# Optimization experiments

Hardware: AMD Instinct MI355X
Metric: run time of the kernel (lower is better)

Reference implementation:

```python
import jax, jax.numpy as jnp
import numpy as np

N, E = 20000, 320000
IN_DIM = OUT_DIM = E_IN = E_OUT = 128
BN_EPS = 1e-5

def _lrelu(x):
    return jnp.where(x >= 0, x, 0.1 * x)

def setup_inputs() -> dict:
    key = jax.random.key(0)
    ks = jax.random.split(key, 12)
    def w(k, shape):
        return jax.random.normal(k, shape, jnp.float32) * (shape[0] ** -0.5)
    return {
        "h": jax.random.normal(ks[0], (N, IN_DIM), jnp.float32),
        "edge_w": jax.random.normal(ks[1], (E, E_IN), jnp.float32),
        "W_node": w(ks[2], (IN_DIM, OUT_DIM)),
        "W_eedge": w(ks[3], (E_IN, E_IN)),
        "W_esf": w(ks[4], (E_IN, 1)),
        "W_fuse": w(ks[5], (2 * OUT_DIM + E_IN, OUT_DIM)),
        "b_fuse": jnp.zeros((OUT_DIM,), jnp.float32),
        "W_attn": w(ks[6], (OUT_DIM, 1)),
        "W_conc": w(ks[7], (2 * OUT_DIM + E_IN, OUT_DIM)),
        "b_conc": jnp.zeros((OUT_DIM,), jnp.float32),
        "bn_gamma": jnp.ones((E_IN,), jnp.float32),
        "bn_beta": jnp.zeros((E_IN,), jnp.float32),
        "W_aggre": w(ks[8], (2 * OUT_DIM + 2 * E_IN, E_OUT)),
        "src": jax.random.randint(ks[9], (E,), 0, N),
        "dst": jax.random.randint(ks[10], (E,), 0, N),
    }

def reference(h, edge_w, W_node, W_eedge, W_esf, W_fuse, b_fuse, W_attn,
              W_conc, b_conc, bn_gamma, bn_beta, W_aggre, src, dst):
    # eval mode: dropout = identity, BatchNorm uses running stats (mean 0, var 1)
    hn = h @ W_node                       # embed_node -> ndata['h'] = ndata['oh']
    # self_attention: ow = embed_edge(w); w = edge_sf_atten(lrelu(ow)) * ow
    ow = edge_w @ W_eedge                 # [E, e_in]
    w1 = (_lrelu(ow) @ W_esf) * ow        # [E, e_in]
    # inter_attention
    hs, hd = hn[src], hn[dst]             # [E, out]
    sat = jnp.concatenate([hs, hd, w1], axis=-1)          # [E, 2*out+e_in]
    inw = _lrelu(sat @ W_fuse + b_fuse)                   # [E, out]
    a = inw @ W_attn                                      # [E, 1]
    w2 = a * w1                                           # edata['w']
    # reduce_func2: segment softmax over incoming edges (grouped by dst)
    s = a[:, 0]
    m = jax.ops.segment_max(s, dst, num_segments=N)
    e = jnp.exp(s - m[dst])
    denom = jax.ops.segment_sum(e, dst, num_segments=N)
    alpha = (e / denom[dst])[:, None]                     # [E, 1]
    t = jnp.concatenate([hs, w2], axis=-1)                # [E, out+e_in]
    h_agg = jax.ops.segment_sum(alpha * t, dst, num_segments=N)  # [N, out+e_in]
    h_new = jnp.concatenate([h_agg, hn], axis=-1) @ W_conc + b_conc
    # DGL only updates nodes that received messages; zero-indegree keep embed_node(h)
    indeg = jax.ops.segment_sum(jnp.ones((E,), jnp.float32), dst, num_segments=N)
    h_out = jnp.where(indeg[:, None] > 0, h_new, hn)      # [N, out]
    # edge_calc: BN(w2) then aggre_embed_edge(cat(src_h, dst_h, bn_w, ow))
    w_bn = (w2 / jnp.sqrt(jnp.float32(1.0) + BN_EPS)) * bn_gamma + bn_beta
    z = jnp.concatenate([h_out[src], h_out[dst], w_bn, ow], axis=-1)
    w_out = z @ W_aggre                                   # [E, e_out]
    return h_out, w_out, sat
```

## Files before the change

### kernel.cpp

```cpp
#include <hip/hip_runtime.h>
#include <hip/hip_bf16.h>

#define TB 256
#define TBM 512
#define BM 64
#define BK 32
#define BN 128
#define ASTR 68
#define MAXD 160

static constexpr int NN = 20000;
static constexpr int NE = 320000;
static constexpr int NB = 313;

static constexpr long long OFF_OW  = 0;
static constexpr long long OFF_HN  = 40960000;
static constexpr long long OFF_PQ  = 43520000;
static constexpr long long OFF_S   = 48640000;
static constexpr long long OFF_DEN = 48960000;
static constexpr long long OFF_CUR = 48980000;
static constexpr long long OFF_WT  = 49000000;
static constexpr long long WS_FLOATS = 49100000;

static constexpr int U_EH = 0;
static constexpr int U_EL = 16384;
static constexpr int U_FH = 32768;
static constexpr int U_FL = 81920;
static constexpr int U_AH = 131072;
static constexpr int U_AL = 163840;

static constexpr long long OUT_HOUT = 0;
static constexpr long long OUT_WOUT = 2560000;
static constexpr long long OUT_SAT  = 43520000;

typedef __attribute__((ext_vector_type(8))) short s8v;
typedef __attribute__((ext_vector_type(4))) float f32x4;
typedef __attribute__((ext_vector_type(8))) unsigned short u16x8;
typedef __attribute__((ext_vector_type(4))) unsigned short u16x4;

#define MFMA16(a,b,c) __builtin_amdgcn_mfma_f32_16x16x32_bf16(a,b,c,0,0,0)

__device__ __forceinline__ float lrelu(float x){ return x >= 0.f ? x : 0.1f*x; }

__device__ __forceinline__ void gl16(const void* g, void* l){
    __builtin_amdgcn_global_load_lds(
        (const __attribute__((address_space(1))) void*)g,
        (__attribute__((address_space(3))) void*)l, 16, 0, 0);
}

__device__ __forceinline__ void split1(float f, unsigned short& hi, unsigned short& lo){
    __hip_bfloat16 h = __float2bfloat16(f);
    float hf = __bfloat162float(h);
    __hip_bfloat16 l = __float2bfloat16(f - hf);
    hi = __builtin_bit_cast(unsigned short, h);
    lo = __builtin_bit_cast(unsigned short, l);
}
__device__ __forceinline__ void split8(float4 a, float4 b, s8v& hi, s8v& lo){
    float v[8] = {a.x,a.y,a.z,a.w,b.x,b.y,b.z,b.w};
#pragma unroll
    for (int j = 0; j < 8; ++j){
        unsigned short hs, ls;
        split1(v[j], hs, ls);
        hi[j] = (short)hs; lo[j] = (short)ls;
    }
}
__device__ __forceinline__ float bfp(unsigned p){
    return __uint_as_float(p & 0xffff0000u) + __uint_as_float(p << 16);
}

__device__ __forceinline__ int lds_a(int row, int g){
    return row*32 + ((g ^ (row & 3)) << 3);
}

__device__ __forceinline__ void store_At(float (*Ast)[ASTR], int k4, int r, float4 v){
    Ast[k4+0][r] = v.x; Ast[k4+1][r] = v.y; Ast[k4+2][r] = v.z; Ast[k4+3][r] = v.w;
}
__device__ __forceinline__ void mm_chunk(const float (*Ast)[ASTR], const float (*Bs)[BN],
                                         int r0, int c0, float acc[4][8]){
#pragma unroll 4
    for (int k = 0; k < BK; ++k){
        const float4 av = *(const float4*)&Ast[k][r0];
        const float4 b0 = *(const float4*)&Bs[k][c0];
        const float4 b1 = *(const float4*)&Bs[k][64 + c0];
        const float a0=av.x, a1=av.y, a2=av.z, a3=av.w;
        const float b[8] = {b0.x,b0.y,b0.z,b0.w,b1.x,b1.y,b1.z,b1.w};
#pragma unroll
        for (int j = 0; j < 8; ++j){
            acc[0][j] = fmaf(a0, b[j], acc[0][j]);
            acc[1][j] = fmaf(a1, b[j], acc[1][j]);
            acc[2][j] = fmaf(a2, b[j], acc[2][j]);
            acc[3][j] = fmaf(a3, b[j], acc[3][j]);
        }
    }
}
__device__ __forceinline__ void load_B(const float* __restrict__ W, int kc,
                                       float (*Bs)[BN], int tid){
#pragma unroll
    for (int p = 0; p < 4; ++p){
        int idx = p*TB + tid;
        int row = idx >> 5;
        int c4  = (idx & 31) << 2;
        *(float4*)&Bs[row][c4] = *(const float4*)&W[(size_t)(kc+row)*BN + c4];
    }
}

__global__ __launch_bounds__(TB) void k_prep(const float* __restrict__ We,
                                             const float* __restrict__ Wf,
                                             const float* __restrict__ Wa,
                                             unsigned short* __restrict__ wt,
                                             int* __restrict__ cur){
    int id = blockIdx.x*TB + threadIdx.x;
    if (id < NN) cur[id] = 0;
    unsigned short hs, ls;
    if (id < 16384){
        int n = id >> 7, k = id & 127;
        split1(We[(size_t)k*128 + n], hs, ls);
        wt[U_EH + id] = hs; wt[U_EL + id] = ls;
    } else if (id < 65536){
        int local = id - 16384;
        int n = local / 384, k = local - n*384;
        split1(Wf[(size_t)k*128 + n], hs, ls);
        wt[U_FH + local] = hs; wt[U_FL + local] = ls;
    } else if (id < 98304){
        int local = id - 65536;
        int n = local >> 8, kk = local & 255;
        split1(Wa[(size_t)(256+kk)*128 + n], hs, ls);
        wt[U_AH + local] = hs; wt[U_AL + local] = ls;
    }
}

__global__ __launch_bounds__(TB) void kB_count(const int* __restrict__ dst,
                                               int* __restrict__ cur){
    int e = blockIdx.x*TB + threadIdx.x;
    atomicAdd(&cur[dst[e]], 1);
}
__global__ __launch_bounds__(TB) void kC_scan(int* __restrict__ cur,
                                              int* __restrict__ offs){
    __shared__ int part[TB];
    __shared__ int spre[TB];
    const int tid = threadIdx.x;
    const int CH = (NN + TB - 1) / TB;
    const int base = tid * CH;
    int sum = 0;
    for (int i = 0; i < CH; ++i){ int idx = base + i; if (idx < NN) sum += cur[idx]; }
    part[tid] = sum;
    __syncthreads();
    if (tid == 0){ int r = 0; for (int i = 0; i < TB; ++i){ spre[i] = r; r += part[i]; } }
    __syncthreads();
    int run = spre[tid];
    for (int i = 0; i < CH; ++i){
        int idx = base + i;
        if (idx < NN){ int c = cur[idx]; offs[idx] = run; cur[idx] = run; run += c; }
    }
}
__global__ __launch_bounds__(TB) void kD_scatter(const int* __restrict__ dst,
                                                 int* __restrict__ cur,
                                                 int* __restrict__ eidx){
    int e = blockIdx.x*TB + threadIdx.x;
    int p = atomicAdd(&cur[dst[e]], 1);
    eidx[p] = e;
}

__global__ __launch_bounds__(TB) void k1_hn(const float* __restrict__ h,
                                            const float* __restrict__ Wn,
                                            unsigned short* __restrict__ hnH,
                                            unsigned short* __restrict__ hnL,
                                            unsigned* __restrict__ hnP){
    __shared__ float Ast[BK][ASTR];
    __shared__ float Bs[BK][BN];
    const int tid = threadIdx.x;
    const int rbase = blockIdx.x * BM;
    const int tc = tid & 15, tr = tid >> 4;
    const int r0 = tr*4, c0 = tc*4;
    float acc[4][8] = {};
    for (int kc = 0; kc < 128; kc += BK){
        __syncthreads();
        {
            int lr = tid >> 3, k4 = (tid & 7) << 2;
#pragma unroll
            for (int p = 0; p < 2; ++p){
                int r = p*32 + lr;
                int rr = rbase + r; if (rr >= NN) rr = NN-1;
                float4 v = *(const float4*)&h[(size_t)rr*128 + kc + k4];
                store_At(Ast, k4, r, v);
            }
        }
        load_B(Wn, kc, Bs, tid);
        __syncthreads();
        mm_chunk(Ast, Bs, r0, c0, acc);
    }
#pragma unroll
    for (int i = 0; i < 4; ++i){
        int rr = rbase + r0 + i;
        if (rr < NN){
            u16x4 h0, l0, h1, l1;
            uint4 p0, p1;
#pragma unroll
            for (int j = 0; j < 4; ++j){
                unsigned short hs, ls;
                split1(acc[i][j], hs, ls);
                h0[j] = hs; l0[j] = ls;
                ((unsigned*)&p0)[j] = ((unsigned)hs << 16) | ls;
                split1(acc[i][4+j], hs, ls);
                h1[j] = hs; l1[j] = ls;
                ((unsigned*)&p1)[j] = ((unsigned)hs << 16) | ls;
            }
            *(u16x4*)&hnH[(size_t)rr*128 + c0] = h0;
            *(u16x4*)&hnL[(size_t)rr*128 + c0] = l0;
            *(u16x4*)&hnH[(size_t)rr*128 + 64 + c0] = h1;
            *(u16x4*)&hnL[(size_t)rr*128 + 64 + c0] = l1;
            *(uint4*)&hnP[(size_t)rr*128 + c0] = p0;
            *(uint4*)&hnP[(size_t)rr*128 + 64 + c0] = p1;
        }
    }
}


__global__ __launch_bounds__(TBM) void k2_mfma(const float* __restrict__ ew,
                                               const unsigned short* __restrict__ wtH,
                                               const unsigned short* __restrict__ wtL,
                                               const float* __restrict__ Wesf,
                                               unsigned short* __restrict__ owH,
                                               unsigned short* __restrict__ owL,
                                               float* __restrict__ sat){
    __shared__ __align__(16) unsigned short Ah[2][4096], Al[2][4096], Bh[2][4096], Bl[2][4096];
    __shared__ float sEsf[128];
    const int tid = threadIdx.x;
    const long long rbase = (long long)blockIdx.x * 128;
    const int lane = tid & 63, w = tid >> 6;
    const int ls = lane & 15, lg = lane >> 4;
    const int srow = tid >> 2, sg = tid & 3;
    const int gsw = sg ^ (srow & 3);
    const int aslot = srow*32 + (gsw << 3);
    if (tid < 128) sEsf[tid] = Wesf[tid];
    f32x4 acc[8] = {};
    auto stage = [&](int nb, int t){
        const int kc = t*32;
        gl16(&wtH[srow*128 + kc + gsw*8], &Bh[nb][w*512]);
        gl16(&wtL[srow*128 + kc + gsw*8], &Bl[nb][w*512]);
        const float* p = &ew[(rbase + srow)*128 + kc + sg*8];
        float4 v0 = *(const float4*)p, v1 = *(const float4*)(p+4);
        s8v hi, lo; split8(v0, v1, hi, lo);
        *(s8v*)&Ah[nb][aslot] = hi; *(s8v*)&Al[nb][aslot] = lo;
    };
    stage(0, 0);
    __syncthreads();
    int cur = 0;
    for (int t = 0; t < 4; ++t){
        if (t+1 < 4) stage(cur^1, t+1);
        s8v ah = *(const s8v*)&Ah[cur][lds_a(w*16 + ls, lg)];
        s8v al = *(const s8v*)&Al[cur][lds_a(w*16 + ls, lg)];
#pragma unroll
        for (int ct = 0; ct < 8; ++ct){
            int c = ct*16 + ls;
            s8v bh = *(const s8v*)&Bh[cur][lds_a(c,lg)];
            s8v bl = *(const s8v*)&Bl[cur][lds_a(c,lg)];
            acc[ct] = MFMA16(ah, bh, acc[ct]);
            acc[ct] = MFMA16(ah, bl, acc[ct]);
            acc[ct] = MFMA16(al, bh, acc[ct]);
        }
        __syncthreads();
        cur ^= 1;
    }
#pragma unroll
    for (int reg = 0; reg < 4; ++reg){
        float p = 0.f;
#pragma unroll
        for (int ct = 0; ct < 8; ++ct)
            p += lrelu(acc[ct][reg]) * sEsf[ct*16 + ls];
#pragma unroll
        for (int m = 1; m < 16; m <<= 1) p += __shfl_xor(p, m);
        long long orow = rbase + w*16 + lg*4 + reg;
#pragma unroll
        for (int ct = 0; ct < 8; ++ct){
            float o = acc[ct][reg];
            int col = ct*16 + ls;
            sat[orow*384 + 256 + col] = p * o;
            unsigned short hs_, ls_; split1(o, hs_, ls_);
            owH[orow*128 + col] = hs_;
            owL[orow*128 + col] = ls_;
        }
    }
}

__global__ __launch_bounds__(TBM) void k3_mfma(const unsigned short* __restrict__ hnH,
                                               const unsigned short* __restrict__ hnL,
                                               const unsigned* __restrict__ hnP,
                                               const unsigned short* __restrict__ wtH,
                                               const unsigned short* __restrict__ wtL,
                                               const float* __restrict__ bf,
                                               const float* __restrict__ Wattn,
                                               const int* __restrict__ src,
                                               const int* __restrict__ dst,
                                               float* __restrict__ sat,
                                               float* __restrict__ s_ws){
    __shared__ __align__(16) unsigned short Ah[2][4096], Al[2][4096], Bh[2][4096], Bl[2][4096];
    __shared__ float sBf[128], sAtt[128];
    __shared__ int sSrc[128], sDst[128];
    const int tid = threadIdx.x;
    const long long rbase = (long long)blockIdx.x * 128;
    const int lane = tid & 63, w = tid >> 6;
    const int ls = lane & 15, lg = lane >> 4;
    const int srow = tid >> 2, sg = tid & 3;
    const int gsw = sg ^ (srow & 3);
    const int aslot = srow*32 + (gsw << 3);
    if (tid < 128){
        sBf[tid] = bf[tid]; sAtt[tid] = Wattn[tid];
        sSrc[tid] = src[rbase + tid]; sDst[tid] = dst[rbase + tid];
    }
    __syncthreads();
    f32x4 acc[8] = {};
    auto stage = [&](int nb, int t){
        const int kc = t*32;
        gl16(&wtH[srow*384 + kc + gsw*8], &Bh[nb][w*512]);
        gl16(&wtL[srow*384 + kc + gsw*8], &Bl[nb][w*512]);
        long long e = rbase + srow;
        if (kc < 256){
            int node = (kc < 128) ? sSrc[srow] : sDst[srow];
            int col0 = kc & 127;
            gl16(&hnH[(size_t)node*128 + col0 + gsw*8], &Ah[nb][w*512]);
            gl16(&hnL[(size_t)node*128 + col0 + gsw*8], &Al[nb][w*512]);
            const unsigned* pp = &hnP[(size_t)node*128 + col0 + sg*8];
            uint4 q0 = *(const uint4*)pp, q1 = *(const uint4*)(pp+4);
            float4 v0 = {bfp(q0.x), bfp(q0.y), bfp(q0.z), bfp(q0.w)};
            float4 v1 = {bfp(q1.x), bfp(q1.y), bfp(q1.z), bfp(q1.w)};
            *(float4*)&sat[e*384 + kc + sg*8] = v0;
            *(float4*)&sat[e*384 + kc + sg*8 + 4] = v1;
        } else {
            const float* p = &sat[e*384 + kc + sg*8];
            float4 v0 = *(const float4*)p, v1 = *(const float4*)(p+4);
            s8v hi, lo; split8(v0, v1, hi, lo);
            *(s8v*)&Ah[nb][aslot] = hi; *(s8v*)&Al[nb][aslot] = lo;
        }
    };
    stage(0, 0);
    __syncthreads();
    int cur = 0;
    for (int t = 0; t < 12; ++t){
        if (t+1 < 12) stage(cur^1, t+1);
        s8v ah = *(const s8v*)&Ah[cur][lds_a(w*16 + ls, lg)];
        s8v al = *(const s8v*)&Al[cur][lds_a(w*16 + ls, lg)];
#pragma unroll
        for (int ct = 0; ct < 8; ++ct){
            int c = ct*16 + ls;
            s8v bh = *(const s8v*)&Bh[cur][lds_a(c,lg)];
            s8v bl = *(const s8v*)&Bl[cur][lds_a(c,lg)];
            acc[ct] = MFMA16(ah, bh, acc[ct]);
            acc[ct] = MFMA16(ah, bl, acc[ct]);
            acc[ct] = MFMA16(al, bh, acc[ct]);
        }
        __syncthreads();
        cur ^= 1;
    }
#pragma unroll
    for (int reg = 0; reg < 4; ++reg){
        float p = 0.f;
#pragma unroll
        for (int ct = 0; ct < 8; ++ct){
            int col = ct*16 + ls;
            p += lrelu(acc[ct][reg] + sBf[col]) * sAtt[col];
        }
#pragma unroll
        for (int m = 1; m < 16; m <<= 1) p += __shfl_xor(p, m);
        if (ls == 0) s_ws[rbase + w*16 + lg*4 + reg] = p;
    }
}

__global__ __launch_bounds__(TB) void k5_agg(const float* __restrict__ s,
                                             const unsigned* __restrict__ hnP,
                                             const float* __restrict__ sat,
                                             const int* __restrict__ src,
                                             const int* __restrict__ eidx,
                                             const int* __restrict__ offs,
                                             const int* __restrict__ cur,
                                             float* __restrict__ hagg,
                                             float* __restrict__ den){
    __shared__ int   sEu[4][MAXD];
    __shared__ int   sEs[4][MAXD];
    __shared__ float sAl[4][MAXD];
    __shared__ float sWc[4][MAXD];
    const int wv = threadIdx.x >> 6, lane = threadIdx.x & 63;
    const int n = blockIdx.x*4 + wv;
    int* Eu = sEu[wv]; int* Es = sEs[wv];
    float* Al = sAl[wv]; float* Wc = sWc[wv];
    const int start = offs[n];
    const int deg = cur[n] - start;
    const int dc = deg < MAXD ? deg : MAXD;
    for (int i = lane; i < dc; i += 64) Eu[i] = eidx[start+i];
    __syncthreads();
    for (int i = lane; i < dc; i += 64){
        int my = Eu[i], r = 0;
        for (int j = 0; j < dc; ++j) r += (Eu[j] < my);
        Es[r] = my;
    }
    __syncthreads();
    float lm = -3.402823466e38f;
    for (int i = lane; i < dc; i += 64){
        int e = Es[i];
        float sv = s[e];
        Wc[i] = sv;
        Eu[i] = src[e];
        lm = fmaxf(lm, sv);
    }
    for (int i = MAXD + lane; i < deg; i += 64) lm = fmaxf(lm, s[eidx[start+i]]);
#pragma unroll
    for (int m2 = 32; m2; m2 >>= 1) lm = fmaxf(lm, __shfl_xor(lm, m2));
    const float m = lm;
    float lsum = 0.f;
    for (int i = lane; i < dc; i += 64){
        float ev = expf(Wc[i] - m);
        Al[i] = ev;
        lsum += ev;
    }
    for (int i = MAXD + lane; i < deg; i += 64) lsum += expf(s[eidx[start+i]] - m);
#pragma unroll
    for (int m2 = 32; m2; m2 >>= 1) lsum += __shfl_xor(lsum, m2);
    const float denom = lsum;
    const float inv = (deg > 0) ? 1.f/denom : 0.f;
    for (int i = lane; i < dc; i += 64){
        float al = Al[i] * inv;
        Al[i] = al;
        Wc[i] = al * Wc[i];
    }
    __syncthreads();
    float a0=0.f, a1=0.f, a2=0.f, a3=0.f;
    for (int i = 0; i < dc; ++i){
        int sI = Eu[i];
        size_t e = (size_t)Es[i];
        float al = Al[i], wc = Wc[i];
        unsigned p0 = hnP[(size_t)sI*128 + lane];
        unsigned p1 = hnP[(size_t)sI*128 + 64 + lane];
        float w0 = sat[e*384 + 256 + lane];
        float w1v = sat[e*384 + 256 + 64 + lane];
        a0 = fmaf(al, bfp(p0), a0);
        a1 = fmaf(al, bfp(p1), a1);
        a2 = fmaf(wc, w0, a2);
        a3 = fmaf(wc, w1v, a3);
    }
    for (int i = MAXD; i < deg; ++i){
        int e = eidx[start+i];
        float sv = s[e];
        float al = expf(sv - m) * inv;
        float wc = al * sv;
        int sI = src[e];
        a0 = fmaf(al, bfp(hnP[(size_t)sI*128 + lane]), a0);
        a1 = fmaf(al, bfp(hnP[(size_t)sI*128 + 64 + lane]), a1);
        a2 = fmaf(wc, sat[(size_t)e*384 + 256 + lane], a2);
        a3 = fmaf(wc, sat[(size_t)e*384 + 256 + 64 + lane], a3);
    }
    const size_t b = (size_t)n*256;
    hagg[b + lane] = a0;
    hagg[b + 64 + lane] = a1;
    hagg[b + 128 + lane] = a2;
    hagg[b + 192 + lane] = a3;
    if (lane == 0) den[n] = (deg > 0) ? denom : 0.f;
}

__global__ __launch_bounds__(TB) void k6_conc(const float* __restrict__ hagg,
                                              const unsigned* __restrict__ hnP,
                                              const float* __restrict__ Wc,
                                              const float* __restrict__ bc,
                                              const float* __restrict__ den,
                                              float* __restrict__ hout){
    __shared__ float Ast[BK][ASTR];
    __shared__ float Bs[BK][BN];
    __shared__ float sBc[BN];
    const int tid = threadIdx.x;
    const int rbase = blockIdx.x * BM;
    const int tc = tid & 15, tr = tid >> 4;
    const int r0 = tr*4, c0 = tc*4;
    if (tid < BN) sBc[tid] = bc[tid];
    float acc[4][8] = {};
    for (int chunk = 0; chunk < 12; ++chunk){
        int kc = chunk * BK;
        __syncthreads();
        {
            int lr = tid >> 3, k4 = (tid & 7) << 2;
#pragma unroll
            for (int p = 0; p < 2; ++p){
                int r = p*32 + lr;
                int rr = rbase + r; if (rr >= NN) rr = NN-1;
                float4 v;
                if (chunk < 8) v = *(const float4*)&hagg[(size_t)rr*256 + kc + k4];
                else {
                    int cb = (kc - 256) + k4;
                    uint4 q = *(const uint4*)&hnP[(size_t)rr*128 + cb];
                    v.x = bfp(q.x); v.y = bfp(q.y); v.z = bfp(q.z); v.w = bfp(q.w);
                }
                store_At(Ast, k4, r, v);
            }
        }
        load_B(Wc, kc, Bs, tid);
        __syncthreads();
        mm_chunk(Ast, Bs, r0, c0, acc);
    }
#pragma unroll
    for (int i = 0; i < 4; ++i){
        int rr = rbase + r0 + i;
        if (rr >= NN) continue;
        bool keep = den[rr] > 0.f;
        float o[8];
#pragma unroll
        for (int j = 0; j < 8; ++j){
            int col = (j < 4) ? (c0 + j) : (60 + c0 + j);
            float fb = bfp(hnP[(size_t)rr*128 + col]);
            o[j] = keep ? acc[i][j] + sBc[col] : fb;
        }
        float4 o0 = {o[0],o[1],o[2],o[3]}, o1 = {o[4],o[5],o[6],o[7]};
        *(float4*)&hout[(size_t)rr*128 + c0] = o0;
        *(float4*)&hout[(size_t)rr*128 + 64 + c0] = o1;
    }
}

__global__ __launch_bounds__(TB) void kNG(const float* __restrict__ aF,
                                          const float* __restrict__ W,
                                          float* __restrict__ O){
    __shared__ float Ast[BK][ASTR];
    __shared__ float Bs[BK][BN];
    const int tid = threadIdx.x;
    const int half = blockIdx.x >= NB ? 1 : 0;
    const int rbase = (blockIdx.x - half*NB) * BM;
    const float* Wp = W + (size_t)half*16384;
    const int tc = tid & 15, tr = tid >> 4;
    const int r0 = tr*4, c0 = tc*4;
    float acc[4][8] = {};
    for (int kc = 0; kc < 128; kc += BK){
        __syncthreads();
        {
            int lr = tid >> 3, k4 = (tid & 7) << 2;
#pragma unroll
            for (int p = 0; p < 2; ++p){
                int r = p*32 + lr;
                int rr = rbase + r; if (rr >= NN) rr = NN-1;
                float4 v = *(const float4*)&aF[(size_t)rr*128 + kc + k4];
                store_At(Ast, k4, r, v);
            }
        }
        load_B(Wp, kc, Bs, tid);
        __syncthreads();
        mm_chunk(Ast, Bs, r0, c0, acc);
    }
#pragma unroll
    for (int i = 0; i < 4; ++i){
        int rr = rbase + r0 + i;
        if (rr < NN){
            float4 o0 = {acc[i][0],acc[i][1],acc[i][2],acc[i][3]};
            float4 o1 = {acc[i][4],acc[i][5],acc[i][6],acc[i][7]};
            *(float4*)&O[(size_t)rr*256 + half*128 + c0] = o0;
            *(float4*)&O[(size_t)rr*256 + half*128 + 64 + c0] = o1;
        }
    }
}

__global__ __launch_bounds__(TBM) void k7p(const unsigned short* __restrict__ owH,
                                           const unsigned short* __restrict__ owL,
                                           const float* __restrict__ sarr,
                                           const float* __restrict__ sat,
                                           const float* __restrict__ Q,
                                           const float* __restrict__ gamma,
                                           const float* __restrict__ beta,
                                           const unsigned short* __restrict__ wtH,
                                           const unsigned short* __restrict__ wtL,
                                           const int* __restrict__ src,
                                           const int* __restrict__ dst,
                                           float* __restrict__ w2out){
    __shared__ __align__(16) unsigned short Ah[2][4096], Al[2][4096], Bh[2][4096], Bl[2][4096];
    __shared__ float sGam[128], sBet[128], sS[128];
    __shared__ int sSrc[128], sDst[128];
    const int tid = threadIdx.x;
    const long long rbase = (long long)blockIdx.x * 128;
    const int lane = tid & 63, w = tid >> 6;
    const int ls = lane & 15, lg = lane >> 4;
    const int srow = tid >> 2, sg = tid & 3;
    const int gsw = sg ^ (srow & 3);
    const int aslot = srow*32 + (gsw << 3);
    const float ISR = 0.9999950000374997f;
    if (tid < 128){
        sGam[tid] = gamma[tid] * ISR; sBet[tid] = beta[tid];
        sSrc[tid] = src[rbase + tid]; sDst[tid] = dst[rbase + tid];
        sS[tid] = sarr[rbase + tid];
    }
    __syncthreads();
    f32x4 acc[8] = {};
    auto stage = [&](int nb, int t){
        const int kc = t*32;
        gl16(&wtH[srow*256 + kc + gsw*8], &Bh[nb][w*512]);
        gl16(&wtL[srow*256 + kc + gsw*8], &Bl[nb][w*512]);
        long long e = rbase + srow;
        if (kc < 128){
            int cb = kc + sg*8;
            float se = sS[srow];
            const float* p = &sat[e*384 + 256 + cb];
            float4 v0 = *(const float4*)p, v1 = *(const float4*)(p+4);
            v0.x = fmaf(v0.x*se, sGam[cb+0], sBet[cb+0]);
            v0.y = fmaf(v0.y*se, sGam[cb+1], sBet[cb+1]);
            v0.z = fmaf(v0.z*se, sGam[cb+2], sBet[cb+2]);
            v0.w = fmaf(v0.w*se, sGam[cb+3], sBet[cb+3]);
            v1.x = fmaf(v1.x*se, sGam[cb+4], sBet[cb+4]);
            v1.y = fmaf(v1.y*se, sGam[cb+5], sBet[cb+5]);
            v1.z = fmaf(v1.z*se, sGam[cb+6], sBet[cb+6]);
            v1.w = fmaf(v1.w*se, sGam[cb+7], sBet[cb+7]);
            s8v hi, lo; split8(v0, v1, hi, lo);
            *(s8v*)&Ah[nb][aslot] = hi; *(s8v*)&Al[nb][aslot] = lo;
        } else {
            int col0 = kc - 128;
            gl16(&owH[e*128 + col0 + gsw*8], &Ah[nb][w*512]);
            gl16(&owL[e*128 + col0 + gsw*8], &Al[nb][w*512]);
        }
    };
    stage(0, 0);
    __syncthreads();
    int cur = 0;
    for (int t = 0; t < 8; ++t){
        if (t+1 < 8) stage(cur^1, t+1);
        int r = w*16 + ls;
        s8v ah = *(const s8v*)&Ah[cur][r*32 + ((lg ^ (r&3)) << 3)];
        s8v al = *(const s8v*)&Al[cur][r*32 + ((lg ^ (r&3)) << 3)];
#pragma unroll
        for (int ct = 0; ct < 8; ++ct){
            int c = ct*16 + ls;
            s8v bh = *(const s8v*)&Bh[cur][c*32 + ((lg ^ (c&3)) << 3)];
            s8v bl = *(const s8v*)&Bl[cur][c*32 + ((lg ^ (c&3)) << 3)];
            acc[ct] = MFMA16(ah, bh, acc[ct]);
            acc[ct] = MFMA16(ah, bl, acc[ct]);
            acc[ct] = MFMA16(al, bh, acc[ct]);
        }
        __syncthreads();
        cur ^= 1;
    }
#pragma unroll
    for (int reg = 0; reg < 4; ++reg){
        int row = w*16 + lg*4 + reg;
        long long orow = rbase + row;
        int sI = sSrc[row], dI = sDst[row];
#pragma unroll
        for (int ct = 0; ct < 8; ++ct){
            int col = ct*16 + ls;
            w2out[orow*128 + col] = acc[ct][reg]
                                  + Q[(size_t)sI*256 + col]
                                  + Q[(size_t)dI*256 + 128 + col];
        }
    }
}

extern "C" void kernel_launch(void* const* d_in, const int* in_sizes, int n_in,
                              void* d_out, int out_size, void* d_ws, size_t ws_size,
                              hipStream_t stream){
    (void)in_sizes; (void)n_in; (void)out_size;
    const float* h       = (const float*)d_in[0];
    const float* edge_w  = (const float*)d_in[1];
    const float* W_node  = (const float*)d_in[2];
    const float* W_eedge = (const float*)d_in[3];
    const float* W_esf   = (const float*)d_in[4];
    const float* W_fuse  = (const float*)d_in[5];
    const float* b_fuse  = (const float*)d_in[6];
    const float* W_attn  = (const float*)d_in[7];
    const float* W_conc  = (const float*)d_in[8];
    const float* b_conc  = (const float*)d_in[9];
    const float* gamma   = (const float*)d_in[10];
    const float* beta    = (const float*)d_in[11];
    const float* W_aggre = (const float*)d_in[12];
    const int*   src     = (const int*)d_in[13];
    const int*   dst     = (const int*)d_in[14];

    float* out    = (float*)d_out;
    float* o_hout = out + OUT_HOUT;
    float* o_wout = out + OUT_WOUT;
    float* o_sat  = out + OUT_SAT;

    if (ws_size < (size_t)WS_FLOATS * 4) return;
    float* ws     = (float*)d_ws;
    unsigned short* w_owH = (unsigned short*)(ws + OFF_OW);
    unsigned short* w_owL = w_owH + (size_t)NE*128;
    unsigned short* w_hnH = (unsigned short*)(ws + OFF_HN);
    unsigned short* w_hnL = w_hnH + (size_t)NN*128;
    float* w_PQ   = ws + OFF_PQ;
    float* w_s    = ws + OFF_S;
    float* w_den  = ws + OFF_DEN;
    int*   w_cur  = (int*)(ws + OFF_CUR);
    unsigned short* w_wt = (unsigned short*)(ws + OFF_WT);

    unsigned* w_hnP = (unsigned*)o_wout;
    int* w_eidx = (int*)o_hout;
    int* w_offs = w_eidx + NE;

    hipLaunchKernelGGL(k_prep,    dim3(98304/TB), dim3(TB), 0, stream,
                       W_eedge, W_fuse, W_aggre, w_wt, w_cur);
    hipLaunchKernelGGL(kB_count,  dim3(NE/TB), dim3(TB), 0, stream, dst, w_cur);
    hipLaunchKernelGGL(kC_scan,   dim3(1), dim3(TB), 0, stream, w_cur, w_offs);
    hipLaunchKernelGGL(kD_scatter,dim3(NE/TB), dim3(TB), 0, stream, dst, w_cur, w_eidx);
    hipLaunchKernelGGL(k1_hn,     dim3(NB), dim3(TB), 0, stream, h, W_node,
                       w_hnH, w_hnL, w_hnP);
    hipLaunchKernelGGL(k2_mfma,   dim3(NE/128), dim3(TBM), 0, stream, edge_w,
                       w_wt + U_EH, w_wt + U_EL, W_esf, w_owH, w_owL, o_sat);
    hipLaunchKernelGGL(k3_mfma,   dim3(NE/128), dim3(TBM), 0, stream, w_hnH, w_hnL, w_hnP,
                       w_wt + U_FH, w_wt + U_FL, b_fuse, W_attn,
                       src, dst, o_sat, w_s);
    hipLaunchKernelGGL(k5_agg,    dim3(NN/4), dim3(TB), 0, stream, w_s, w_hnP, o_sat,
                       src, w_eidx, w_offs, w_cur, w_PQ, w_den);
    hipLaunchKernelGGL(k6_conc,   dim3(NB), dim3(TB), 0, stream, w_PQ,
                       w_hnP, W_conc, b_conc, w_den, o_hout);
    hipLaunchKernelGGL(kNG,       dim3(2*NB), dim3(TB), 0, stream, o_hout, W_aggre, w_PQ);
    hipLaunchKernelGGL(k7p,       dim3(NE/128), dim3(TBM), 0, stream,
                       w_owH, w_owL, w_s, o_sat, w_PQ, gamma, beta,
                       w_wt + U_AH, w_wt + U_AL, src, dst, o_wout);
}
```

Before: 726.1 us.

## Fuse edge embedding and fuse-attention GEMMs into one kernel, use wave-level syncs

Merges k2 (edge embed and self-attention) and k3 (fuse-layer GEMM and attention score) into a single kernel. The w1 block now feeds the second GEMM straight from registers into LDS instead of being re-read from the sat output in global memory. The K order of the second GEMM is rotated so the w1 chunks come first. In the aggregation kernel, block barriers are replaced with LDS waitcnt, which assumes each wave only touches its own shared slice. The fused kernel holds more registers (acc1, acc2 and pr live together), which may lower occupancy.

```diff
diff --git a/kernel.cpp b/kernel.cpp
--- a/kernel.cpp
+++ b/kernel.cpp
@@ -35,12 +35,13 @@
 
 typedef __attribute__((ext_vector_type(8))) short s8v;
 typedef __attribute__((ext_vector_type(4))) float f32x4;
-typedef __attribute__((ext_vector_type(8))) unsigned short u16x8;
 typedef __attribute__((ext_vector_type(4))) unsigned short u16x4;
 
 #define MFMA16(a,b,c) __builtin_amdgcn_mfma_f32_16x16x32_bf16(a,b,c,0,0,0)
 
 __device__ __forceinline__ float lrelu(float x){ return x >= 0.f ? x : 0.1f*x; }
+
+__device__ __forceinline__ void wsync(){ asm volatile("s_waitcnt lgkmcnt(0)" ::: "memory"); }
 
 __device__ __forceinline__ void gl16(const void* g, void* l){
     __builtin_amdgcn_global_load_lds(
@@ -215,87 +216,25 @@
     }
 }
 
-
-__global__ __launch_bounds__(TBM) void k2_mfma(const float* __restrict__ ew,
-                                               const unsigned short* __restrict__ wtH,
-                                               const unsigned short* __restrict__ wtL,
-                                               const float* __restrict__ Wesf,
-                                               unsigned short* __restrict__ owH,
-                                               unsigned short* __restrict__ owL,
-                                               float* __restrict__ sat){
+__global__ __launch_bounds__(TBM) void k23_mfma(const float* __restrict__ ew,
+                                                const unsigned short* __restrict__ wtEH,
+                                                const unsigned short* __restrict__ wtEL,
+                                                const float* __restrict__ Wesf,
+                                                const unsigned short* __restrict__ wtFH,
+                                                const unsigned short* __restrict__ wtFL,
+                                                const float* __restrict__ bf,
+                                                const float* __restrict__ Wattn,
+                                                const unsigned short* __restrict__ hnH,
+                                                const unsigned short* __restrict__ hnL,
+                                                const unsigned* __restrict__ hnP,
+                                                const int* __restrict__ src,
+                                                const int* __restrict__ dst,
+                                                unsigned short* __restrict__ owH,
+                                                unsigned short* __restrict__ owL,
+                                                float* __restrict__ sat,
+                                                float* __restrict__ s_ws){
     __shared__ __align__(16) unsigned short Ah[2][4096], Al[2][4096], Bh[2][4096], Bl[2][4096];
-    __shared__ float sEsf[128];
-    const int tid = threadIdx.x;
-    const long long rbase = (long long)blockIdx.x * 128;
-    const int lane = tid & 63, w = tid >> 6;
-    const int ls = lane & 15, lg = lane >> 4;
-    const int srow = tid >> 2, sg = tid & 3;
-    const int gsw = sg ^ (srow & 3);
-    const int aslot = srow*32 + (gsw << 3);
-    if (tid < 128) sEsf[tid] = Wesf[tid];
-    f32x4 acc[8] = {};
-    auto stage = [&](int nb, int t){
-        const int kc = t*32;
-        gl16(&wtH[srow*128 + kc + gsw*8], &Bh[nb][w*512]);
-        gl16(&wtL[srow*128 + kc + gsw*8], &Bl[nb][w*512]);
-        const float* p = &ew[(rbase + srow)*128 + kc + sg*8];
-        float4 v0 = *(const float4*)p, v1 = *(const float4*)(p+4);
-        s8v hi, lo; split8(v0, v1, hi, lo);
-        *(s8v*)&Ah[nb][aslot] = hi; *(s8v*)&Al[nb][aslot] = lo;
-    };
-    stage(0, 0);
-    __syncthreads();
-    int cur = 0;
-    for (int t = 0; t < 4; ++t){
-        if (t+1 < 4) stage(cur^1, t+1);
-        s8v ah = *(const s8v*)&Ah[cur][lds_a(w*16 + ls, lg)];
-        s8v al = *(const s8v*)&Al[cur][lds_a(w*16 + ls, lg)];
-#pragma unroll
-        for (int ct = 0; ct < 8; ++ct){
-            int c = ct*16 + ls;
-            s8v bh = *(const s8v*)&Bh[cur][lds_a(c,lg)];
-            s8v bl = *(const s8v*)&Bl[cur][lds_a(c,lg)];
-            acc[ct] = MFMA16(ah, bh, acc[ct]);
-            acc[ct] = MFMA16(ah, bl, acc[ct]);
-            acc[ct] = MFMA16(al, bh, acc[ct]);
-        }
-        __syncthreads();
-        cur ^= 1;
-    }
-#pragma unroll
-    for (int reg = 0; reg < 4; ++reg){
-        float p = 0.f;
-#pragma unroll
-        for (int ct = 0; ct < 8; ++ct)
-            p += lrelu(acc[ct][reg]) * sEsf[ct*16 + ls];
-#pragma unroll
-        for (int m = 1; m < 16; m <<= 1) p += __shfl_xor(p, m);
-        long long orow = rbase + w*16 + lg*4 + reg;
-#pragma unroll
-        for (int ct = 0; ct < 8; ++ct){
-            float o = acc[ct][reg];
-            int col = ct*16 + ls;
-            sat[orow*384 + 256 + col] = p * o;
-            unsigned short hs_, ls_; split1(o, hs_, ls_);
-            owH[orow*128 + col] = hs_;
-            owL[orow*128 + col] = ls_;
-        }
-    }
-}
-
-__global__ __launch_bounds__(TBM) void k3_mfma(const unsigned short* __restrict__ hnH,
-                                               const unsigned short* __restrict__ hnL,
-                                               const unsigned* __restrict__ hnP,
-                                               const unsigned short* __restrict__ wtH,
-                                               const unsigned short* __restrict__ wtL,
-                                               const float* __restrict__ bf,
-                                               const float* __restrict__ Wattn,
-                                               const int* __restrict__ src,
-                                               const int* __restrict__ dst,
-                                               float* __restrict__ sat,
-                                               float* __restrict__ s_ws){
-    __shared__ __align__(16) unsigned short Ah[2][4096], Al[2][4096], Bh[2][4096], Bl[2][4096];
-    __shared__ float sBf[128], sAtt[128];
+    __shared__ float sEsf[128], sBf[128], sAtt[128];
     __shared__ int sSrc[128], sDst[128];
     const int tid = threadIdx.x;
     const long long rbase = (long long)blockIdx.x * 128;
@@ -305,39 +244,24 @@
     const int gsw = sg ^ (srow & 3);
     const int aslot = srow*32 + (gsw << 3);
     if (tid < 128){
-        sBf[tid] = bf[tid]; sAtt[tid] = Wattn[tid];
+        sEsf[tid] = Wesf[tid]; sBf[tid] = bf[tid]; sAtt[tid] = Wattn[tid];
         sSrc[tid] = src[rbase + tid]; sDst[tid] = dst[rbase + tid];
     }
-    __syncthreads();
-    f32x4 acc[8] = {};
-    auto stage = [&](int nb, int t){
+    f32x4 acc1[8] = {};
+    auto stageA = [&](int nb, int t){
         const int kc = t*32;
-        gl16(&wtH[srow*384 + kc + gsw*8], &Bh[nb][w*512]);
-        gl16(&wtL[srow*384 + kc + gsw*8], &Bl[nb][w*512]);
-        long long e = rbase + srow;
-        if (kc < 256){
-            int node = (kc < 128) ? sSrc[srow] : sDst[srow];
-            int col0 = kc & 127;
-            gl16(&hnH[(size_t)node*128 + col0 + gsw*8], &Ah[nb][w*512]);
-            gl16(&hnL[(size_t)node*128 + col0 + gsw*8], &Al[nb][w*512]);
-            const unsigned* pp = &hnP[(size_t)node*128 + col0 + sg*8];
-            uint4 q0 = *(const uint4*)pp, q1 = *(const uint4*)(pp+4);
-            float4 v0 = {bfp(q0.x), bfp(q0.y), bfp(q0.z), bfp(q0.w)};
-            float4 v1 = {bfp(q1.x), bfp(q1.y), bfp(q1.z), bfp(q1.w)};
-            *(float4*)&sat[e*384 + kc + sg*8] = v0;
-            *(float4*)&sat[e*384 + kc + sg*8 + 4] = v1;
-        } else {
-            const float* p = &sat[e*384 + kc + sg*8];
-            float4 v0 = *(const float4*)p, v1 = *(const float4*)(p+4);
-            s8v hi, lo; split8(v0, v1, hi, lo);
-            *(s8v*)&Ah[nb][aslot] = hi; *(s8v*)&Al[nb][aslot] = lo;
-        }
+        gl16(&wtEH[srow*128 + kc + gsw*8], &Bh[nb][w*512]);
+        gl16(&wtEL[srow*128 + kc + gsw*8], &Bl[nb][w*512]);
+        const float* p = &ew[(rbase + srow)*128 + kc + sg*8];
+        float4 v0 = *(const float4*)p, v1 = *(const float4*)(p+4);
+        s8v hi, lo; split8(v0, v1, hi, lo);
+        *(s8v*)&Ah[nb][aslot] = hi; *(s8v*)&Al[nb][aslot] = lo;
     };
-    stage(0, 0);
+    stageA(0, 0);
     __syncthreads();
     int cur = 0;
-    for (int t = 0; t < 12; ++t){
-        if (t+1 < 12) stage(cur^1, t+1);
+    for (int t = 0; t < 4; ++t){
+        if (t < 3) stageA(cur^1, t+1);
         s8v ah = *(const s8v*)&Ah[cur][lds_a(w*16 + ls, lg)];
         s8v al = *(const s8v*)&Al[cur][lds_a(w*16 + ls, lg)];
 #pragma unroll
@@ -345,20 +269,97 @@
             int c = ct*16 + ls;
             s8v bh = *(const s8v*)&Bh[cur][lds_a(c,lg)];
             s8v bl = *(const s8v*)&Bl[cur][lds_a(c,lg)];
-            acc[ct] = MFMA16(ah, bh, acc[ct]);
-            acc[ct] = MFMA16(ah, bl, acc[ct]);
-            acc[ct] = MFMA16(al, bh, acc[ct]);
+            acc1[ct] = MFMA16(ah, bh, acc1[ct]);
+            acc1[ct] = MFMA16(ah, bl, acc1[ct]);
+            acc1[ct] = MFMA16(al, bh, acc1[ct]);
         }
         __syncthreads();
         cur ^= 1;
     }
+    float pr[4];
 #pragma unroll
     for (int reg = 0; reg < 4; ++reg){
         float p = 0.f;
 #pragma unroll
+        for (int ct = 0; ct < 8; ++ct)
+            p += lrelu(acc1[ct][reg]) * sEsf[ct*16 + ls];
+#pragma unroll
+        for (int m = 1; m < 16; m <<= 1) p += __shfl_xor(p, m);
+        pr[reg] = p;
+        long long orow = rbase + w*16 + lg*4 + reg;
+#pragma unroll
+        for (int ct = 0; ct < 8; ++ct){
+            float o = acc1[ct][reg];
+            int col = ct*16 + ls;
+            sat[orow*384 + 256 + col] = p * o;
+            unsigned short hs_, ls_; split1(o, hs_, ls_);
+            owH[orow*128 + col] = hs_;
+            owL[orow*128 + col] = ls_;
+        }
+    }
+    f32x4 acc2[8] = {};
+    auto stageC = [&](int nb, int t2){
+        const int kb = 256 + t2*32;
+        gl16(&wtFH[srow*384 + kb + gsw*8], &Bh[nb][w*512]);
+        gl16(&wtFL[srow*384 + kb + gsw*8], &Bl[nb][w*512]);
+#pragma unroll
+        for (int q = 0; q < 2; ++q){
+            int ct = 2*t2 + q;
+#pragma unroll
+            for (int reg = 0; reg < 4; ++reg){
+                int row = w*16 + lg*4 + reg;
+                int col = ct*16 + ls;
+                int kl = col - t2*32;
+                int g = kl >> 3;
+                int base = row*32 + ((g ^ (row & 3)) << 3) + (kl & 7);
+                unsigned short hh, ll; split1(pr[reg] * acc1[ct][reg], hh, ll);
+                Ah[nb][base] = hh;
+                Al[nb][base] = ll;
+            }
+        }
+    };
+    auto stageD = [&](int nb, int t3){
+        const int kc = t3*32;
+        gl16(&wtFH[srow*384 + kc + gsw*8], &Bh[nb][w*512]);
+        gl16(&wtFL[srow*384 + kc + gsw*8], &Bl[nb][w*512]);
+        long long e = rbase + srow;
+        int node = (kc < 128) ? sSrc[srow] : sDst[srow];
+        int col0 = kc & 127;
+        gl16(&hnH[(size_t)node*128 + col0 + gsw*8], &Ah[nb][w*512]);
+        gl16(&hnL[(size_t)node*128 + col0 + gsw*8], &Al[nb][w*512]);
+        const unsigned* pp = &hnP[(size_t)node*128 + col0 + sg*8];
+        uint4 q0 = *(const uint4*)pp, q1 = *(const uint4*)(pp+4);
+        float4 v0 = {bfp(q0.x), bfp(q0.y), bfp(q0.z), bfp(q0.w)};
+        float4 v1 = {bfp(q1.x), bfp(q1.y), bfp(q1.z), bfp(q1.w)};
+        *(float4*)&sat[e*384 + kc + sg*8] = v0;
+        *(float4*)&sat[e*384 + kc + sg*8 + 4] = v1;
+    };
+    auto stage2 = [&](int nb, int u){ if (u < 4) stageC(nb, u); else stageD(nb, u - 4); };
+    stage2(cur, 0);
+    __syncthreads();
+    for (int u = 0; u < 12; ++u){
+        if (u < 11) stage2(cur^1, u+1);
+        s8v ah = *(const s8v*)&Ah[cur][lds_a(w*16 + ls, lg)];
+        s8v al = *(const s8v*)&Al[cur][lds_a(w*16 + ls, lg)];
+#pragma unroll
+        for (int ct = 0; ct < 8; ++ct){
+            int c = ct*16 + ls;
+            s8v bh = *(const s8v*)&Bh[cur][lds_a(c,lg)];
+            s8v bl = *(const s8v*)&Bl[cur][lds_a(c,lg)];
+            acc2[ct] = MFMA16(ah, bh, acc2[ct]);
+            acc2[ct] = MFMA16(ah, bl, acc2[ct]);
+            acc2[ct] = MFMA16(al, bh, acc2[ct]);
+        }
+        __syncthreads();
+        cur ^= 1;
+    }
+#pragma unroll
+    for (int reg = 0; reg < 4; ++reg){
+        float p = 0.f;
+#pragma unroll
         for (int ct = 0; ct < 8; ++ct){
             int col = ct*16 + ls;
-            p += lrelu(acc[ct][reg] + sBf[col]) * sAtt[col];
+            p += lrelu(acc2[ct][reg] + sBf[col]) * sAtt[col];
         }
 #pragma unroll
         for (int m = 1; m < 16; m <<= 1) p += __shfl_xor(p, m);
@@ -387,13 +388,13 @@
     const int deg = cur[n] - start;
     const int dc = deg < MAXD ? deg : MAXD;
     for (int i = lane; i < dc; i += 64) Eu[i] = eidx[start+i];
-    __syncthreads();
+    wsync();
     for (int i = lane; i < dc; i += 64){
         int my = Eu[i], r = 0;
         for (int j = 0; j < dc; ++j) r += (Eu[j] < my);
         Es[r] = my;
     }
-    __syncthreads();
+    wsync();
     float lm = -3.402823466e38f;
     for (int i = lane; i < dc; i += 64){
         int e = Es[i];
@@ -406,6 +407,7 @@
 #pragma unroll
     for (int m2 = 32; m2; m2 >>= 1) lm = fmaxf(lm, __shfl_xor(lm, m2));
     const float m = lm;
+    wsync();
     float lsum = 0.f;
     for (int i = lane; i < dc; i += 64){
         float ev = expf(Wc[i] - m);
@@ -422,7 +424,7 @@
         Al[i] = al;
         Wc[i] = al * Wc[i];
     }
-    __syncthreads();
+    wsync();
     float a0=0.f, a1=0.f, a2=0.f, a3=0.f;
     for (int i = 0; i < dc; ++i){
         int sI = Eu[i];
@@ -691,11 +693,11 @@
     hipLaunchKernelGGL(kD_scatter,dim3(NE/TB), dim3(TB), 0, stream, dst, w_cur, w_eidx);
     hipLaunchKernelGGL(k1_hn,     dim3(NB), dim3(TB), 0, stream, h, W_node,
                        w_hnH, w_hnL, w_hnP);
-    hipLaunchKernelGGL(k2_mfma,   dim3(NE/128), dim3(TBM), 0, stream, edge_w,
-                       w_wt + U_EH, w_wt + U_EL, W_esf, w_owH, w_owL, o_sat);
-    hipLaunchKernelGGL(k3_mfma,   dim3(NE/128), dim3(TBM), 0, stream, w_hnH, w_hnL, w_hnP,
+    hipLaunchKernelGGL(k23_mfma,  dim3(NE/128), dim3(TBM), 0, stream, edge_w,
+                       w_wt + U_EH, w_wt + U_EL, W_esf,
                        w_wt + U_FH, w_wt + U_FL, b_fuse, W_attn,
-                       src, dst, o_sat, w_s);
+                       w_hnH, w_hnL, w_hnP, src, dst,
+                       w_owH, w_owL, o_sat, w_s);
     hipLaunchKernelGGL(k5_agg,    dim3(NN/4), dim3(TB), 0, stream, w_s, w_hnP, o_sat,
                        src, w_eidx, w_offs, w_cur, w_PQ, w_den);
     hipLaunchKernelGGL(k6_conc,   dim3(NB), dim3(TB), 0, stream, w_PQ,
```

After: 698.9 us. 1.04x faster.
